# Optimization experiments

Measured on AMD Instinct MI355X. Metric: run time of the kernel, lower is better.

## Reference

```python
import jax, jax.numpy as jnp
import numpy as np

NUM_HEADS = 4
HIDDEN = 128
LN_EPS = 1e-6
NEG_INF = -1e9


def setup_inputs() -> dict:
    key = jax.random.key(0)
    ks = jax.random.split(key, 8)
    B, S, H, NH = 64, 512, HIDDEN, NUM_HEADS
    enc = jax.random.normal(ks[0], (B, S, H), dtype=jnp.float32)
    mask = jax.random.randint(ks[1], (B, 1, S, S), 0, 2, dtype=jnp.int32)
    scale = 1.0 / np.sqrt(H)
    # torch Linear(H, H*NH, bias=False): weight is (H*NH, H); store transposed (H, H*NH)
    Wq = jax.random.normal(ks[2], (H, H * NH), dtype=jnp.float32) * scale
    Wk = jax.random.normal(ks[3], (H, H * NH), dtype=jnp.float32) * scale
    Wv = jax.random.normal(ks[4], (H, H * NH), dtype=jnp.float32) * scale
    Wo = jax.random.normal(ks[5], (H * NH, H), dtype=jnp.float32) * (1.0 / np.sqrt(H * NH))
    gamma = jnp.ones((H,), dtype=jnp.float32)
    beta = jnp.zeros((H,), dtype=jnp.float32)
    return {"enc": enc, "mask": mask, "Wq": Wq, "Wk": Wk, "Wv": Wv, "Wo": Wo, "gamma": gamma, "beta": beta}


def reference(enc, mask, Wq, Wk, Wv, Wo, gamma, beta):
    B, S, H = enc.shape
    NH = NUM_HEADS
    # projections -> (B, NH, S, H): each head has head_dim == hidden_units
    Q = (enc @ Wq).reshape(B, S, NH, H).transpose(0, 2, 1, 3)
    K = (enc @ Wk).reshape(B, S, NH, H).transpose(0, 2, 1, 3)
    V = (enc @ Wv).reshape(B, S, NH, H).transpose(0, 2, 1, 3)
    # scaled dot-product attention with mask (non-flash: full score matrix)
    scores = jnp.einsum('bhqd,bhkd->bhqk', Q, K) / jnp.sqrt(jnp.float32(H))
    scores = jnp.where(mask == 0, jnp.float32(NEG_INF), scores)
    attn = jax.nn.softmax(scores, axis=-1)  # dropout = identity in eval mode
    ctx = jnp.einsum('bhqk,bhkd->bhqd', attn, V)  # (B, NH, S, H)
    ctx = ctx.transpose(0, 2, 1, 3).reshape(B, S, NH * H)
    out = ctx @ Wo + enc  # dropout identity, residual add
    # LayerNorm over last dim
    mu = jnp.mean(out, axis=-1, keepdims=True)
    var = jnp.var(out, axis=-1, keepdims=True)
    return gamma * (out - mu) / jnp.sqrt(var + LN_EPS) + beta
```

## Files before the change

kernel.cpp:

```cpp
#include <hip/hip_runtime.h>
#include <stdint.h>

#define BATCH 64
#define SLEN 512
#define HID 128
#define NHEAD 4
#define DPROJ 512
#define MTOT (BATCH * SLEN)
#define SCALE 0.08838834764831845f
#define LOG2E 1.4426950408889634f

using short8 = __attribute__((ext_vector_type(8))) short;
using f32x4  = __attribute__((ext_vector_type(4))) float;
using u32x4  = __attribute__((ext_vector_type(4))) unsigned int;
using u32x2  = __attribute__((ext_vector_type(2))) unsigned int;
using us4    = __attribute__((ext_vector_type(4))) unsigned short;

__device__ __forceinline__ unsigned short f2bf(float f) {
  unsigned int u = __float_as_uint(f);
  u += 0x7fffu + ((u >> 16) & 1u);
  return (unsigned short)(u >> 16);
}

__global__ __launch_bounds__(256) void prep_kernel(
    const float* __restrict__ Wq,
    const float* __restrict__ Wk,
    const float* __restrict__ Wv,
    const float* __restrict__ Wo,
    const float* __restrict__ enc,
    const int* __restrict__ mask,
    unsigned short* __restrict__ WT,
    unsigned short* __restrict__ WoT,
    unsigned short* __restrict__ encb,
    unsigned int* __restrict__ mbits)
{
  if (blockIdx.x < 1024) {
    int idx = blockIdx.x * 256 + threadIdx.x;
    int z = idx >> 16;
    int i = idx & 65535;
    if (z < 3) {
      const float* W = (z == 0) ? Wq : (z == 1) ? Wk : Wv;
      float scale = (z == 0) ? (SCALE * LOG2E) : 1.0f;
      int k = i >> 9;
      int n = i & 511;
      WT[(size_t)z * 65536 + (size_t)n * 128 + k] = f2bf(W[i] * scale);
    } else {
      int k = i >> 7;
      int n = i & 127;
      WoT[(size_t)n * 512 + k] = f2bf(Wo[i]);
    }
  } else if (blockIdx.x < 3072) {
    size_t tid = (size_t)(blockIdx.x - 1024) * 256 + threadIdx.x;
    const float* s = enc + tid * 8;
    f32x4 a0 = *(const f32x4*)(s);
    f32x4 a1 = *(const f32x4*)(s + 4);
    short8 v;
    #pragma unroll
    for (int j = 0; j < 4; ++j) v[j] = (short)f2bf(a0[j]);
    #pragma unroll
    for (int j = 0; j < 4; ++j) v[4 + j] = (short)f2bf(a1[j]);
    *(short8*)(encb + tid * 8) = v;
  } else {
    const int l = threadIdx.x & 63;
    const int wv = threadIdx.x >> 6;
    const int m = blockIdx.x - 3072;
    #pragma unroll 4
    for (int it = 0; it < 16; ++it) {
      size_t tile = (size_t)m * 64 + (size_t)wv * 16 + it;
      u32x4 v = *(const u32x4*)(mask + tile * 256 + l * 4);
      unsigned nib = (v[0] ? 1u : 0u) | (v[1] ? 2u : 0u) |
                     (v[2] ? 4u : 0u) | (v[3] ? 8u : 0u);
      unsigned a  = nib | ((unsigned)__shfl_xor((int)nib, 1, 64) << 4);
      unsigned b2 = a   | ((unsigned)__shfl_xor((int)a,   2, 64) << 8);
      unsigned c  = b2  | ((unsigned)__shfl_xor((int)b2,  4, 64) << 16);
      if ((l & 7) == 0) mbits[tile * 8 + (l >> 3)] = c;
    }
  }
}

__global__ __launch_bounds__(256) void qkv_kernel(
    const unsigned short* __restrict__ encb,
    const unsigned short* __restrict__ WT,
    unsigned short* __restrict__ Qh,
    unsigned short* __restrict__ Kh,
    unsigned short* __restrict__ Vt)
{
  const int nt = blockIdx.x;
  const int mt = blockIdx.y;
  const int t = threadIdx.x;
  const int lane = t & 63;
  const int w = t >> 6;
  const int quad = lane >> 4;
  const int l16 = lane & 15;

  __shared__ __align__(16) unsigned short Ald[128 * 136];
  __shared__ __align__(16) unsigned short Bld[2][128 * 72];

  const int m0 = mt * 128, n0 = nt * 128;
  const int wm = (w >> 1) * 64, wn = (w & 1) * 64;

  const int b_row = t >> 3, b_col = (t & 7) << 3;

  {
    u32x4 areg[8];
    #pragma unroll
    for (int i = 0; i < 8; ++i) {
      int idx = i * 256 + t;
      areg[i] = *(const u32x4*)(encb + (size_t)(m0 + (idx >> 4)) * HID + ((idx & 15) << 3));
    }
    u32x4 breg0[4];
    #pragma unroll
    for (int i = 0; i < 4; ++i)
      breg0[i] = *(const u32x4*)(WT + (size_t)(n0 + b_row + i * 32) * HID + b_col);
    #pragma unroll
    for (int i = 0; i < 8; ++i) {
      int idx = i * 256 + t;
      *(u32x4*)(Ald + (idx >> 4) * 136 + ((idx & 15) << 3)) = areg[i];
    }
    #pragma unroll
    for (int i = 0; i < 4; ++i)
      *(u32x4*)(Bld[0] + (b_row + i * 32) * 72 + b_col) = breg0[i];
  }
  u32x4 breg[4];
  #pragma unroll
  for (int i = 0; i < 4; ++i)
    breg[i] = *(const u32x4*)(WT + (size_t)(n0 + b_row + i * 32) * HID + 64 + b_col);
  asm volatile("s_waitcnt lgkmcnt(0)" ::: "memory");
  __builtin_amdgcn_s_barrier();

  f32x4 acc[4][4];
  #pragma unroll
  for (int s = 0; s < 6; ++s) {
    const int z = s >> 1, kc = s & 1, p = s & 1;
    if (kc == 0) {
      #pragma unroll
      for (int mi = 0; mi < 4; ++mi)
        #pragma unroll
        for (int ni = 0; ni < 4; ++ni)
          acc[mi][ni] = f32x4{0.f, 0.f, 0.f, 0.f};
    }

    const unsigned short* Br = Bld[p];
    #pragma unroll
    for (int kk = 0; kk < 2; ++kk) {
      short8 a[4], bb[4];
      #pragma unroll
      for (int mi = 0; mi < 4; ++mi)
        a[mi] = *(const short8*)(Ald + (wm + mi * 16 + l16) * 136 + kc * 64 + kk * 32 + quad * 8);
      #pragma unroll
      for (int ni = 0; ni < 4; ++ni)
        bb[ni] = *(const short8*)(Br + (wn + ni * 16 + l16) * 72 + kk * 32 + quad * 8);
      if (z < 2) {
        #pragma unroll
        for (int mi = 0; mi < 4; ++mi)
          #pragma unroll
          for (int ni = 0; ni < 4; ++ni)
            acc[mi][ni] = __builtin_amdgcn_mfma_f32_16x16x32_bf16(bb[ni], a[mi], acc[mi][ni], 0, 0, 0);
      } else {
        #pragma unroll
        for (int mi = 0; mi < 4; ++mi)
          #pragma unroll
          for (int ni = 0; ni < 4; ++ni)
            acc[mi][ni] = __builtin_amdgcn_mfma_f32_16x16x32_bf16(a[mi], bb[ni], acc[mi][ni], 0, 0, 0);
      }
    }

    if (s < 5) {
      unsigned short* Bw2 = Bld[p ^ 1];
      #pragma unroll
      for (int i = 0; i < 4; ++i)
        *(u32x4*)(Bw2 + (b_row + i * 32) * 72 + b_col) = breg[i];
      if (s < 4) {
        const int s2 = s + 2;
        const unsigned short* Wz = WT + (size_t)(s2 >> 1) * DPROJ * HID;
        #pragma unroll
        for (int i = 0; i < 4; ++i)
          breg[i] = *(const u32x4*)(Wz + (size_t)(n0 + b_row + i * 32) * HID + (s2 & 1) * 64 + b_col);
      }
      asm volatile("s_waitcnt lgkmcnt(0)" ::: "memory");
      __builtin_amdgcn_s_barrier();
    }

    if (kc == 1) {
      if (z < 2) {
        unsigned short* outz = ((z == 0) ? Qh : Kh) + (size_t)nt * MTOT * HID;
        #pragma unroll
        for (int mi = 0; mi < 4; ++mi)
          #pragma unroll
          for (int ni = 0; ni < 4; ++ni) {
            int m = m0 + wm + mi * 16 + l16;
            int dbase = wn + ni * 16 + quad * 4;
            us4 pk;
            #pragma unroll
            for (int r = 0; r < 4; ++r) pk[r] = f2bf(acc[mi][ni][r]);
            *(us4*)(outz + (size_t)m * HID + dbase) = pk;
          }
      } else {
        #pragma unroll
        for (int mi = 0; mi < 4; ++mi)
          #pragma unroll
          for (int ni = 0; ni < 4; ++ni) {
            int row0 = m0 + wm + mi * 16 + quad * 4;
            int b = row0 >> 9, sres = row0 & 511;
            int d = wn + ni * 16 + l16;
            us4 pk;
            #pragma unroll
            for (int r = 0; r < 4; ++r) pk[r] = f2bf(acc[mi][ni][r]);
            *(us4*)(Vt + ((size_t)(nt * BATCH + b) * HID + d) * SLEN + sres) = pk;
          }
      }
    }
  }
}

__global__ __launch_bounds__(512, 4) void attn_kernel(
    const unsigned short* __restrict__ Qh,
    const unsigned short* __restrict__ Kh,
    const unsigned short* __restrict__ Vt,
    const unsigned int* __restrict__ mbits,
    unsigned short* __restrict__ ctx)
{
  const int lin = blockIdx.x;
  const int work = (lin & 7) * 128 + (lin >> 3);
  const int qt = work & 3;
  const int h  = (work >> 2) & 3;
  const int b  = work >> 4;

  const int t = threadIdx.x;
  const int lane = t & 63;
  const int w = t >> 6;
  const int quad = lane >> 4;
  const int l16 = lane & 15;

  __shared__ __align__(16) unsigned short Kld[2][64 * 136];
  __shared__ __align__(16) unsigned short Vtld[2][128 * 72];

  const int q0 = qt * 128;
  const size_t rowbase = (size_t)b * SLEN;
  const unsigned short* kbase0 = Kh + ((size_t)h * MTOT + rowbase) * HID;
  const unsigned short* vbase  = Vt + (size_t)(h * BATCH + b) * HID * SLEN;
  const unsigned int* mrow = mbits + (size_t)b * SLEN * 16;

  const int k_key = t >> 4, k_col = (t & 15) << 3;
  const int v_d   = t >> 3, v_cc  = (t & 7) << 3;

  short8 qa[4];
  {
    const unsigned short* qbase =
        Qh + ((size_t)h * MTOT + rowbase + q0 + w * 16 + l16) * HID + quad * 8;
    #pragma unroll
    for (int kk = 0; kk < 4; ++kk)
      qa[kk] = *(const short8*)(qbase + kk * 32);
  }

  short8 ones;
  #pragma unroll
  for (int j = 0; j < 8; ++j) ones[j] = (short)0x3F80;

  f32x4 oc[8], oc9;
  #pragma unroll
  for (int nd = 0; nd < 8; ++nd) oc[nd] = f32x4{0.f, 0.f, 0.f, 0.f};
  oc9 = f32x4{0.f, 0.f, 0.f, 0.f};

  const unsigned int* mq = mrow + (size_t)(q0 + w * 16 + l16) * 16;

  u32x4 kreg[2], vreg[2];
  #pragma unroll
  for (int i = 0; i < 2; ++i) {
    kreg[i] = *(const u32x4*)(kbase0 + (size_t)(k_key + i * 32) * HID + k_col);
    vreg[i] = *(const u32x4*)(vbase + (size_t)(v_d + i * 64) * SLEN + v_cc);
  }
  #pragma unroll
  for (int i = 0; i < 2; ++i) {
    *(u32x4*)(Kld[0] + (k_key + i * 32) * 136 + k_col) = kreg[i];
    *(u32x4*)(Vtld[0] + (v_d + i * 64) * 72 + v_cc) = vreg[i];
  }
  #pragma unroll
  for (int i = 0; i < 2; ++i) {
    kreg[i] = *(const u32x4*)(kbase0 + (size_t)(64 + k_key + i * 32) * HID + k_col);
    vreg[i] = *(const u32x4*)(vbase + (size_t)(v_d + i * 64) * SLEN + 64 + v_cc);
  }
  asm volatile("s_waitcnt lgkmcnt(0)" ::: "memory");
  __builtin_amdgcn_s_barrier();

  for (int c0 = 0; c0 < SLEN; c0 += 64) {
    const int p = (c0 >> 6) & 1;
    const unsigned short* Kr = Kld[p];
    const unsigned short* Vr = Vtld[p];

    if (c0 + 64 < SLEN) {
      unsigned short* Kw = Kld[p ^ 1];
      unsigned short* Vw = Vtld[p ^ 1];
      #pragma unroll
      for (int i = 0; i < 2; ++i) {
        *(u32x4*)(Kw + (k_key + i * 32) * 136 + k_col) = kreg[i];
        *(u32x4*)(Vw + (v_d + i * 64) * 72 + v_cc) = vreg[i];
      }
      if (c0 + 128 < SLEN) {
        #pragma unroll
        for (int i = 0; i < 2; ++i) {
          kreg[i] = *(const u32x4*)(kbase0 + (size_t)(c0 + 128 + k_key + i * 32) * HID + k_col);
          vreg[i] = *(const u32x4*)(vbase + (size_t)(v_d + i * 64) * SLEN + c0 + 128 + v_cc);
        }
      }
    }

    u32x2 mw = *(const u32x2*)(mq + (c0 >> 5));

    f32x4 sc[4];
    #pragma unroll
    for (int ni = 0; ni < 4; ++ni) sc[ni] = f32x4{0.f, 0.f, 0.f, 0.f};
    __builtin_amdgcn_s_setprio(1);
    #pragma unroll
    for (int kk = 0; kk < 4; ++kk) {
      #pragma unroll
      for (int ni = 0; ni < 4; ++ni) {
        short8 bb = *(const short8*)(Kr + (ni * 16 + l16) * 136 + kk * 32 + quad * 8);
        sc[ni] = __builtin_amdgcn_mfma_f32_16x16x32_bf16(bb, qa[kk], sc[ni], 0, 0, 0);
      }
    }
    __builtin_amdgcn_s_setprio(0);

    unsigned int pk[4][2];
    #pragma unroll
    for (int ni = 0; ni < 4; ++ni) {
      unsigned wsel = (ni < 2) ? mw[0] : mw[1];
      float pp[4];
      #pragma unroll
      for (int r = 0; r < 4; ++r) {
        int bit = (ni & 1) * 16 + quad * 4 + r;
        float e = __builtin_amdgcn_exp2f(sc[ni][r]);
        pp[r] = ((wsel >> bit) & 1u) ? e : 0.f;
      }
      asm("v_cvt_pk_bf16_f32 %0, %1, %2" : "=v"(pk[ni][0]) : "v"(pp[0]), "v"(pp[1]));
      asm("v_cvt_pk_bf16_f32 %0, %1, %2" : "=v"(pk[ni][1]) : "v"(pp[2]), "v"(pp[3]));
    }

    #pragma unroll
    for (int kb = 0; kb < 2; ++kb) {
      unsigned int c0w = pk[kb * 2][0], c2w = pk[kb * 2 + 1][0];
      asm("v_permlane32_swap_b32 %0, %1" : "+v"(c0w), "+v"(c2w));
      asm("v_permlane16_swap_b32 %0, %1" : "+v"(c0w), "+v"(c2w));
      unsigned int c1w = pk[kb * 2][1], c3w = pk[kb * 2 + 1][1];
      asm("v_permlane32_swap_b32 %0, %1" : "+v"(c1w), "+v"(c3w));
      asm("v_permlane16_swap_b32 %0, %1" : "+v"(c1w), "+v"(c3w));
      short8 a = __builtin_bit_cast(short8, u32x4{c0w, c1w, c2w, c3w});
      __builtin_amdgcn_s_setprio(1);
      #pragma unroll
      for (int nd = 0; nd < 8; ++nd) {
        short8 bv = *(const short8*)(Vr + (nd * 16 + l16) * 72 + kb * 32 + quad * 8);
        oc[nd] = __builtin_amdgcn_mfma_f32_16x16x32_bf16(a, bv, oc[nd], 0, 0, 0);
      }
      oc9 = __builtin_amdgcn_mfma_f32_16x16x32_bf16(a, ones, oc9, 0, 0, 0);
      __builtin_amdgcn_s_setprio(0);
    }

    if (c0 + 64 < SLEN) {
      asm volatile("s_waitcnt lgkmcnt(0)" ::: "memory");
      __builtin_amdgcn_s_barrier();
    }
  }

  float rcp[4];
  #pragma unroll
  for (int r = 0; r < 4; ++r) rcp[r] = __builtin_amdgcn_rcpf(oc9[r]);
  #pragma unroll
  for (int nd = 0; nd < 8; ++nd)
    #pragma unroll
    for (int r = 0; r < 4; ++r) {
      float val = oc[nd][r] * rcp[r];
      int row = q0 + w * 16 + quad * 4 + r;
      int col = h * HID + nd * 16 + l16;
      ctx[(rowbase + row) * DPROJ + col] = f2bf(val);
    }
}

__global__ __launch_bounds__(256, 2) void oproj_ln_kernel(
    const unsigned short* __restrict__ ctx,
    const unsigned short* __restrict__ WoT,
    const float* __restrict__ enc,
    const float* __restrict__ gamma,
    const float* __restrict__ beta,
    float* __restrict__ out)
{
  const int m0 = blockIdx.x * 64;
  const int t = threadIdx.x;
  const int lane = t & 63;
  const int w = t >> 6;
  const int quad = lane >> 4;
  const int l16 = lane & 15;

  __shared__ __align__(16) unsigned short Actx[2][64 * 72];
  __shared__ __align__(16) unsigned short Bw[2][128 * 72];

  const int a_row = t >> 3, a_col = (t & 7) << 3;
  const int b_row = t >> 3, b_col = (t & 7) << 3;

  f32x4 acc[8];
  #pragma unroll
  for (int ni = 0; ni < 8; ++ni) acc[ni] = f32x4{0.f, 0.f, 0.f, 0.f};

  u32x4 areg[2], breg[4];
  #pragma unroll
  for (int i = 0; i < 2; ++i)
    areg[i] = *(const u32x4*)(ctx + (size_t)(m0 + a_row + i * 32) * DPROJ + a_col);
  #pragma unroll
  for (int i = 0; i < 4; ++i)
    breg[i] = *(const u32x4*)(WoT + (size_t)(b_row + i * 32) * DPROJ + b_col);
  #pragma unroll
  for (int i = 0; i < 2; ++i)
    *(u32x4*)(Actx[0] + (a_row + i * 32) * 72 + a_col) = areg[i];
  #pragma unroll
  for (int i = 0; i < 4; ++i)
    *(u32x4*)(Bw[0] + (b_row + i * 32) * 72 + b_col) = breg[i];
  #pragma unroll
  for (int i = 0; i < 2; ++i)
    areg[i] = *(const u32x4*)(ctx + (size_t)(m0 + a_row + i * 32) * DPROJ + 64 + a_col);
  #pragma unroll
  for (int i = 0; i < 4; ++i)
    breg[i] = *(const u32x4*)(WoT + (size_t)(b_row + i * 32) * DPROJ + 64 + b_col);
  asm volatile("s_waitcnt lgkmcnt(0)" ::: "memory");
  __builtin_amdgcn_s_barrier();

  #pragma unroll
  for (int it = 0; it < 8; ++it) {
    const int p = it & 1;
    const unsigned short* Ar = Actx[p];
    const unsigned short* Br = Bw[p];
    #pragma unroll
    for (int kk = 0; kk < 2; ++kk) {
      short8 a = *(const short8*)(Ar + (w * 16 + l16) * 72 + kk * 32 + quad * 8);
      #pragma unroll
      for (int ni = 0; ni < 8; ++ni) {
        short8 bb = *(const short8*)(Br + (ni * 16 + l16) * 72 + kk * 32 + quad * 8);
        acc[ni] = __builtin_amdgcn_mfma_f32_16x16x32_bf16(a, bb, acc[ni], 0, 0, 0);
      }
    }
    if (it < 7) {
      unsigned short* Aw2 = Actx[p ^ 1];
      unsigned short* Bw2 = Bw[p ^ 1];
      #pragma unroll
      for (int i = 0; i < 2; ++i)
        *(u32x4*)(Aw2 + (a_row + i * 32) * 72 + a_col) = areg[i];
      #pragma unroll
      for (int i = 0; i < 4; ++i)
        *(u32x4*)(Bw2 + (b_row + i * 32) * 72 + b_col) = breg[i];
      if (it < 6) {
        const int kc2 = (it + 2) * 64;
        #pragma unroll
        for (int i = 0; i < 2; ++i)
          areg[i] = *(const u32x4*)(ctx + (size_t)(m0 + a_row + i * 32) * DPROJ + kc2 + a_col);
        #pragma unroll
        for (int i = 0; i < 4; ++i)
          breg[i] = *(const u32x4*)(WoT + (size_t)(b_row + i * 32) * DPROJ + kc2 + b_col);
      }
      asm volatile("s_waitcnt lgkmcnt(0)" ::: "memory");
      __builtin_amdgcn_s_barrier();
    }
  }

  float g[8], be[8];
  #pragma unroll
  for (int ni = 0; ni < 8; ++ni) {
    g[ni] = gamma[ni * 16 + l16];
    be[ni] = beta[ni * 16 + l16];
  }

  float val[8][4];
  #pragma unroll
  for (int r = 0; r < 4; ++r) {
    int m = m0 + w * 16 + quad * 4 + r;
    const float* erow = enc + (size_t)m * HID;
    float s = 0.f, s2 = 0.f;
    #pragma unroll
    for (int ni = 0; ni < 8; ++ni) {
      float v = acc[ni][r] + erow[ni * 16 + l16];
      val[ni][r] = v;
      s += v;
      s2 += v * v;
    }
    #pragma unroll
    for (int off = 1; off < 16; off <<= 1) {
      s  += __shfl_xor(s, off, 64);
      s2 += __shfl_xor(s2, off, 64);
    }
    float mean = s * (1.f / 128.f);
    float var = s2 * (1.f / 128.f) - mean * mean;
    float rstd = rsqrtf(var + 1e-6f);
    float* orow = out + (size_t)m * HID;
    #pragma unroll
    for (int ni = 0; ni < 8; ++ni)
      orow[ni * 16 + l16] = g[ni] * (val[ni][r] - mean) * rstd + be[ni];
  }
}

extern "C" void kernel_launch(void* const* d_in, const int* in_sizes, int n_in,
                              void* d_out, int out_size, void* d_ws, size_t ws_size,
                              hipStream_t stream) {
  const float* enc   = (const float*)d_in[0];
  const int*   mask  = (const int*)d_in[1];
  const float* Wq    = (const float*)d_in[2];
  const float* Wk    = (const float*)d_in[3];
  const float* Wv    = (const float*)d_in[4];
  const float* Wo    = (const float*)d_in[5];
  const float* gamma = (const float*)d_in[6];
  const float* beta  = (const float*)d_in[7];
  float* out = (float*)d_out;

  unsigned short* WT  = (unsigned short*)d_ws;
  unsigned short* WoT = WT + (size_t)3 * DPROJ * HID;
  unsigned short* Qh  = WoT + (size_t)HID * DPROJ;
  unsigned short* Kh  = Qh + (size_t)NHEAD * MTOT * HID;
  unsigned short* Vt  = Kh + (size_t)NHEAD * MTOT * HID;
  unsigned short* ctx = Vt + (size_t)NHEAD * MTOT * HID;
  unsigned short* encb = ctx + (size_t)MTOT * DPROJ;
  unsigned int* mbits = (unsigned int*)(encb + (size_t)MTOT * HID);

  prep_kernel<<<4096, 256, 0, stream>>>(Wq, Wk, Wv, Wo, enc, mask, WT, WoT, encb, mbits);
  qkv_kernel<<<dim3(4, 256), 256, 0, stream>>>(encb, WT, Qh, Kh, Vt);
  attn_kernel<<<1024, 512, 0, stream>>>(Qh, Kh, Vt, mbits, ctx);
  oproj_ln_kernel<<<MTOT / 64, 256, 0, stream>>>(ctx, WoT, enc, gamma, beta, out);
}
```

Measured before the change: 225.3 us.

## Give each attention wave two 16-row query tiles to reuse K/V LDS reads

The attention kernel now launches 256 threads per block instead of 512, and each wave handles 32 query rows as two 16-row MFMA tiles. Every K and V fragment read from LDS feeds two MFMAs, which halves LDS read traffic per unit of math. The V global prefetch is moved after the QK MFMAs to spread out load issue. In exchange, register pressure roughly doubles for accumulators and Q fragments, which may lower occupancy (launch bounds 256,2), and each thread now stages twice as much data into LDS.

```diff
diff --git a/kernel.cpp b/kernel.cpp
--- a/kernel.cpp
+++ b/kernel.cpp
@@ -213,7 +213,7 @@
   }
 }
 
-__global__ __launch_bounds__(512, 4) void attn_kernel(
+__global__ __launch_bounds__(256, 2) void attn_kernel(
     const unsigned short* __restrict__ Qh,
     const unsigned short* __restrict__ Kh,
     const unsigned short* __restrict__ Vt,
@@ -244,41 +244,46 @@
   const int k_key = t >> 4, k_col = (t & 15) << 3;
   const int v_d   = t >> 3, v_cc  = (t & 7) << 3;
 
-  short8 qa[4];
-  {
+  short8 qa[2][4];
+  #pragma unroll
+  for (int mi = 0; mi < 2; ++mi) {
     const unsigned short* qbase =
-        Qh + ((size_t)h * MTOT + rowbase + q0 + w * 16 + l16) * HID + quad * 8;
+        Qh + ((size_t)h * MTOT + rowbase + q0 + w * 32 + mi * 16 + l16) * HID + quad * 8;
     #pragma unroll
     for (int kk = 0; kk < 4; ++kk)
-      qa[kk] = *(const short8*)(qbase + kk * 32);
+      qa[mi][kk] = *(const short8*)(qbase + kk * 32);
   }
 
   short8 ones;
   #pragma unroll
   for (int j = 0; j < 8; ++j) ones[j] = (short)0x3F80;
 
-  f32x4 oc[8], oc9;
-  #pragma unroll
-  for (int nd = 0; nd < 8; ++nd) oc[nd] = f32x4{0.f, 0.f, 0.f, 0.f};
-  oc9 = f32x4{0.f, 0.f, 0.f, 0.f};
-
-  const unsigned int* mq = mrow + (size_t)(q0 + w * 16 + l16) * 16;
-
-  u32x4 kreg[2], vreg[2];
-  #pragma unroll
-  for (int i = 0; i < 2; ++i) {
-    kreg[i] = *(const u32x4*)(kbase0 + (size_t)(k_key + i * 32) * HID + k_col);
-    vreg[i] = *(const u32x4*)(vbase + (size_t)(v_d + i * 64) * SLEN + v_cc);
-  }
-  #pragma unroll
-  for (int i = 0; i < 2; ++i) {
-    *(u32x4*)(Kld[0] + (k_key + i * 32) * 136 + k_col) = kreg[i];
-    *(u32x4*)(Vtld[0] + (v_d + i * 64) * 72 + v_cc) = vreg[i];
-  }
-  #pragma unroll
-  for (int i = 0; i < 2; ++i) {
-    kreg[i] = *(const u32x4*)(kbase0 + (size_t)(64 + k_key + i * 32) * HID + k_col);
-    vreg[i] = *(const u32x4*)(vbase + (size_t)(v_d + i * 64) * SLEN + 64 + v_cc);
+  f32x4 oc[2][8], oc9[2];
+  #pragma unroll
+  for (int mi = 0; mi < 2; ++mi) {
+    #pragma unroll
+    for (int nd = 0; nd < 8; ++nd) oc[mi][nd] = f32x4{0.f, 0.f, 0.f, 0.f};
+    oc9[mi] = f32x4{0.f, 0.f, 0.f, 0.f};
+  }
+
+  const unsigned int* mq0 = mrow + (size_t)(q0 + w * 32 + l16) * 16;
+  const unsigned int* mq1 = mq0 + 256;
+
+  u32x4 kreg[4], vreg[4];
+  #pragma unroll
+  for (int i = 0; i < 4; ++i) {
+    kreg[i] = *(const u32x4*)(kbase0 + (size_t)(k_key + i * 16) * HID + k_col);
+    vreg[i] = *(const u32x4*)(vbase + (size_t)(v_d + i * 32) * SLEN + v_cc);
+  }
+  #pragma unroll
+  for (int i = 0; i < 4; ++i) {
+    *(u32x4*)(Kld[0] + (k_key + i * 16) * 136 + k_col) = kreg[i];
+    *(u32x4*)(Vtld[0] + (v_d + i * 32) * 72 + v_cc) = vreg[i];
+  }
+  #pragma unroll
+  for (int i = 0; i < 4; ++i) {
+    kreg[i] = *(const u32x4*)(kbase0 + (size_t)(64 + k_key + i * 16) * HID + k_col);
+    vreg[i] = *(const u32x4*)(vbase + (size_t)(v_d + i * 32) * SLEN + 64 + v_cc);
   }
   asm volatile("s_waitcnt lgkmcnt(0)" ::: "memory");
   __builtin_amdgcn_s_barrier();
@@ -292,68 +297,86 @@
       unsigned short* Kw = Kld[p ^ 1];
       unsigned short* Vw = Vtld[p ^ 1];
       #pragma unroll
-      for (int i = 0; i < 2; ++i) {
-        *(u32x4*)(Kw + (k_key + i * 32) * 136 + k_col) = kreg[i];
-        *(u32x4*)(Vw + (v_d + i * 64) * 72 + v_cc) = vreg[i];
+      for (int i = 0; i < 4; ++i) {
+        *(u32x4*)(Kw + (k_key + i * 16) * 136 + k_col) = kreg[i];
+        *(u32x4*)(Vw + (v_d + i * 32) * 72 + v_cc) = vreg[i];
       }
       if (c0 + 128 < SLEN) {
         #pragma unroll
-        for (int i = 0; i < 2; ++i) {
-          kreg[i] = *(const u32x4*)(kbase0 + (size_t)(c0 + 128 + k_key + i * 32) * HID + k_col);
-          vreg[i] = *(const u32x4*)(vbase + (size_t)(v_d + i * 64) * SLEN + c0 + 128 + v_cc);
-        }
-      }
-    }
-
-    u32x2 mw = *(const u32x2*)(mq + (c0 >> 5));
-
-    f32x4 sc[4];
-    #pragma unroll
-    for (int ni = 0; ni < 4; ++ni) sc[ni] = f32x4{0.f, 0.f, 0.f, 0.f};
+        for (int i = 0; i < 4; ++i)
+          kreg[i] = *(const u32x4*)(kbase0 + (size_t)(c0 + 128 + k_key + i * 16) * HID + k_col);
+      }
+    }
+
+    u32x2 mw0 = *(const u32x2*)(mq0 + (c0 >> 5));
+    u32x2 mw1 = *(const u32x2*)(mq1 + (c0 >> 5));
+
+    f32x4 sc[2][4];
+    #pragma unroll
+    for (int mi = 0; mi < 2; ++mi)
+      #pragma unroll
+      for (int ni = 0; ni < 4; ++ni) sc[mi][ni] = f32x4{0.f, 0.f, 0.f, 0.f};
     __builtin_amdgcn_s_setprio(1);
     #pragma unroll
     for (int kk = 0; kk < 4; ++kk) {
       #pragma unroll
       for (int ni = 0; ni < 4; ++ni) {
         short8 bb = *(const short8*)(Kr + (ni * 16 + l16) * 136 + kk * 32 + quad * 8);
-        sc[ni] = __builtin_amdgcn_mfma_f32_16x16x32_bf16(bb, qa[kk], sc[ni], 0, 0, 0);
+        sc[0][ni] = __builtin_amdgcn_mfma_f32_16x16x32_bf16(bb, qa[0][kk], sc[0][ni], 0, 0, 0);
+        sc[1][ni] = __builtin_amdgcn_mfma_f32_16x16x32_bf16(bb, qa[1][kk], sc[1][ni], 0, 0, 0);
       }
     }
     __builtin_amdgcn_s_setprio(0);
 
-    unsigned int pk[4][2];
-    #pragma unroll
-    for (int ni = 0; ni < 4; ++ni) {
-      unsigned wsel = (ni < 2) ? mw[0] : mw[1];
-      float pp[4];
-      #pragma unroll
-      for (int r = 0; r < 4; ++r) {
-        int bit = (ni & 1) * 16 + quad * 4 + r;
-        float e = __builtin_amdgcn_exp2f(sc[ni][r]);
-        pp[r] = ((wsel >> bit) & 1u) ? e : 0.f;
-      }
-      asm("v_cvt_pk_bf16_f32 %0, %1, %2" : "=v"(pk[ni][0]) : "v"(pp[0]), "v"(pp[1]));
-      asm("v_cvt_pk_bf16_f32 %0, %1, %2" : "=v"(pk[ni][1]) : "v"(pp[2]), "v"(pp[3]));
-    }
-
+    if (c0 + 128 < SLEN) {
+      #pragma unroll
+      for (int i = 0; i < 4; ++i)
+        vreg[i] = *(const u32x4*)(vbase + (size_t)(v_d + i * 32) * SLEN + c0 + 128 + v_cc);
+    }
+
+    short8 aF[2][2];
+    #pragma unroll
+    for (int mi = 0; mi < 2; ++mi) {
+      u32x2 mw = (mi == 0) ? mw0 : mw1;
+      unsigned int pk[4][2];
+      #pragma unroll
+      for (int ni = 0; ni < 4; ++ni) {
+        unsigned wsel = (ni < 2) ? mw[0] : mw[1];
+        float pp[4];
+        #pragma unroll
+        for (int r = 0; r < 4; ++r) {
+          int bit = (ni & 1) * 16 + quad * 4 + r;
+          float e = __builtin_amdgcn_exp2f(sc[mi][ni][r]);
+          pp[r] = ((wsel >> bit) & 1u) ? e : 0.f;
+        }
+        asm("v_cvt_pk_bf16_f32 %0, %1, %2" : "=v"(pk[ni][0]) : "v"(pp[0]), "v"(pp[1]));
+        asm("v_cvt_pk_bf16_f32 %0, %1, %2" : "=v"(pk[ni][1]) : "v"(pp[2]), "v"(pp[3]));
+      }
+      #pragma unroll
+      for (int kb = 0; kb < 2; ++kb) {
+        unsigned int c0w = pk[kb * 2][0], c2w = pk[kb * 2 + 1][0];
+        asm("v_permlane32_swap_b32 %0, %1" : "+v"(c0w), "+v"(c2w));
+        asm("v_permlane16_swap_b32 %0, %1" : "+v"(c0w), "+v"(c2w));
+        unsigned int c1w = pk[kb * 2][1], c3w = pk[kb * 2 + 1][1];
+        asm("v_permlane32_swap_b32 %0, %1" : "+v"(c1w), "+v"(c3w));
+        asm("v_permlane16_swap_b32 %0, %1" : "+v"(c1w), "+v"(c3w));
+        aF[mi][kb] = __builtin_bit_cast(short8, u32x4{c0w, c1w, c2w, c3w});
+      }
+    }
+
+    __builtin_amdgcn_s_setprio(1);
     #pragma unroll
     for (int kb = 0; kb < 2; ++kb) {
-      unsigned int c0w = pk[kb * 2][0], c2w = pk[kb * 2 + 1][0];
-      asm("v_permlane32_swap_b32 %0, %1" : "+v"(c0w), "+v"(c2w));
-      asm("v_permlane16_swap_b32 %0, %1" : "+v"(c0w), "+v"(c2w));
-      unsigned int c1w = pk[kb * 2][1], c3w = pk[kb * 2 + 1][1];
-      asm("v_permlane32_swap_b32 %0, %1" : "+v"(c1w), "+v"(c3w));
-      asm("v_permlane16_swap_b32 %0, %1" : "+v"(c1w), "+v"(c3w));
-      short8 a = __builtin_bit_cast(short8, u32x4{c0w, c1w, c2w, c3w});
-      __builtin_amdgcn_s_setprio(1);
       #pragma unroll
       for (int nd = 0; nd < 8; ++nd) {
         short8 bv = *(const short8*)(Vr + (nd * 16 + l16) * 72 + kb * 32 + quad * 8);
-        oc[nd] = __builtin_amdgcn_mfma_f32_16x16x32_bf16(a, bv, oc[nd], 0, 0, 0);
-      }
-      oc9 = __builtin_amdgcn_mfma_f32_16x16x32_bf16(a, ones, oc9, 0, 0, 0);
-      __builtin_amdgcn_s_setprio(0);
-    }
+        oc[0][nd] = __builtin_amdgcn_mfma_f32_16x16x32_bf16(aF[0][kb], bv, oc[0][nd], 0, 0, 0);
+        oc[1][nd] = __builtin_amdgcn_mfma_f32_16x16x32_bf16(aF[1][kb], bv, oc[1][nd], 0, 0, 0);
+      }
+      oc9[0] = __builtin_amdgcn_mfma_f32_16x16x32_bf16(aF[0][kb], ones, oc9[0], 0, 0, 0);
+      oc9[1] = __builtin_amdgcn_mfma_f32_16x16x32_bf16(aF[1][kb], ones, oc9[1], 0, 0, 0);
+    }
+    __builtin_amdgcn_s_setprio(0);
 
     if (c0 + 64 < SLEN) {
       asm volatile("s_waitcnt lgkmcnt(0)" ::: "memory");
@@ -361,18 +384,21 @@
     }
   }
 
-  float rcp[4];
-  #pragma unroll
-  for (int r = 0; r < 4; ++r) rcp[r] = __builtin_amdgcn_rcpf(oc9[r]);
-  #pragma unroll
-  for (int nd = 0; nd < 8; ++nd)
-    #pragma unroll
-    for (int r = 0; r < 4; ++r) {
-      float val = oc[nd][r] * rcp[r];
-      int row = q0 + w * 16 + quad * 4 + r;
-      int col = h * HID + nd * 16 + l16;
-      ctx[(rowbase + row) * DPROJ + col] = f2bf(val);
-    }
+  #pragma unroll
+  for (int mi = 0; mi < 2; ++mi) {
+    float rcp[4];
+    #pragma unroll
+    for (int r = 0; r < 4; ++r) rcp[r] = __builtin_amdgcn_rcpf(oc9[mi][r]);
+    #pragma unroll
+    for (int nd = 0; nd < 8; ++nd)
+      #pragma unroll
+      for (int r = 0; r < 4; ++r) {
+        float val = oc[mi][nd][r] * rcp[r];
+        int row = q0 + w * 32 + mi * 16 + quad * 4 + r;
+        int col = h * HID + nd * 16 + l16;
+        ctx[(rowbase + row) * DPROJ + col] = f2bf(val);
+      }
+  }
 }
 
 __global__ __launch_bounds__(256, 2) void oproj_ln_kernel(
@@ -518,6 +544,6 @@
 
   prep_kernel<<<4096, 256, 0, stream>>>(Wq, Wk, Wv, Wo, enc, mask, WT, WoT, encb, mbits);
   qkv_kernel<<<dim3(4, 256), 256, 0, stream>>>(encb, WT, Qh, Kh, Vt);
-  attn_kernel<<<1024, 512, 0, stream>>>(Qh, Kh, Vt, mbits, ctx);
+  attn_kernel<<<1024, 256, 0, stream>>>(Qh, Kh, Vt, mbits, ctx);
   oproj_ln_kernel<<<MTOT / 64, 256, 0, stream>>>(ctx, WoT, enc, gamma, beta, out);
 }
```

Result: no change. 224.9 us (-0.2%).
